# Optimization experiments

Measured on AMD Instinct MI355X. Metric: run time of the kernel, lower is better.

Reference implementation:

```python
import jax, jax.numpy as jnp
import numpy as np

H = 48       # query heads
KVH = 8      # kv heads (GQA)
G = H // KVH # groups = 6
D = 128      # head_dim
HID = 6144
ROPE_THETA = 1e6


def setup_inputs() -> dict:
    key = jax.random.key(0)
    k1, k2, k3 = jax.random.split(key, 3)
    x = jax.random.normal(k1, (2, 2048, HID), dtype=jnp.float32)
    Wqkv = jax.random.normal(k2, (8192, HID), dtype=jnp.float32) * 0.02
    Wo = jax.random.normal(k3, (HID, HID), dtype=jnp.float32) * 0.02
    return {"x": x, "Wqkv": Wqkv, "Wo": Wo}


def _rotate_half(u):
    return jnp.concatenate([-u[..., D // 2:], u[..., :D // 2]], axis=-1)


def reference(x, Wqkv, Wo):
    B, S, _ = x.shape
    # fused QKV projection, InternLM2 packed layout [B,S,KVH,2+G,D]
    qkv = jnp.einsum('bsh,oh->bso', x, Wqkv).reshape(B, S, KVH, G + 2, D)
    q = qkv[..., :G, :].reshape(B, S, H, D)   # [B,S,H,D]
    k = qkv[..., G, :]                        # [B,S,KVH,D]
    v = qkv[..., G + 1, :]                    # [B,S,KVH,D]

    # RoPE (rotate-half style, theta=1e6)
    inv_freq = 1.0 / (ROPE_THETA ** (jnp.arange(0, D, 2, dtype=jnp.float32) / D))
    freqs = jnp.outer(jnp.arange(S, dtype=jnp.float32), inv_freq)  # [S, D/2]
    emb = jnp.concatenate([freqs, freqs], axis=-1)                 # [S, D]
    cos = jnp.cos(emb)[None, :, None, :]
    sin = jnp.sin(emb)[None, :, None, :]
    q = q * cos + _rotate_half(q) * sin
    k = k * cos + _rotate_half(k) * sin

    # GQA: expand kv heads to query heads
    k = jnp.repeat(k, G, axis=2)  # [B,S,H,D]
    v = jnp.repeat(v, G, axis=2)

    scale = jnp.float32(1.0 / np.sqrt(D))
    scores = jnp.einsum('bqhd,bkhd->bhqk', q, k) * scale  # [B,H,S,S]
    causal = jnp.tril(jnp.ones((S, S), dtype=bool))
    scores = jnp.where(causal[None, None], scores, jnp.float32(-1e30))
    attn = jax.nn.softmax(scores, axis=-1)
    ctx = jnp.einsum('bhqk,bkhd->bqhd', attn, v).reshape(B, S, HID)
    return jnp.einsum('bsh,oh->bso', ctx, Wo)
```

## Files before the change

### kernel.cpp

```cpp
#include <hip/hip_runtime.h>
#include <stdint.h>
#include <stddef.h>


typedef unsigned short u16;
typedef __attribute__((ext_vector_type(8))) short short8;
typedef __attribute__((ext_vector_type(4))) float f32x4;
typedef __attribute__((ext_vector_type(4))) unsigned short u16x4;

typedef const __attribute__((address_space(1))) void* as1_cvp;
typedef __attribute__((address_space(3))) void* as3_vp;

__device__ __forceinline__ float bf2f(u16 u) {
  union { unsigned int i; float f; } v; v.i = ((unsigned)u) << 16; return v.f;
}
__device__ __forceinline__ u16 f2bf(float f) {
  union { float f; unsigned int i; } v; v.f = f;
  unsigned r = v.i + 0x7FFFu + ((v.i >> 16) & 1u);
  return (u16)(r >> 16);
}
__device__ __forceinline__ void gload_lds16(const void* g, void* l) {
  __builtin_amdgcn_global_load_lds((as1_cvp)g, (as3_vp)l, 16, 0, 0);
}

__global__ __launch_bounds__(256) void k_f2bf(const float* __restrict__ in,
                                              u16* __restrict__ out) {
  size_t i = ((size_t)blockIdx.x * 256 + threadIdx.x) * 4;
  f32x4 v = *(const f32x4*)(in + i);
  u16x4 o;
  o[0] = f2bf(v[0]); o[1] = f2bf(v[1]); o[2] = f2bf(v[2]); o[3] = f2bf(v[3]);
  *(u16x4*)(out + i) = o;
}

__device__ __forceinline__ void stage_region(const u16* __restrict__ G,
                                             int K, int kt,
                                             u16 (* __restrict__ XS)[64],
                                             int rmap, int w, int lane) {
  #pragma unroll
  for (int L = 0; L < 2; ++L) {
    const int g = w * 2 + L;
    int rb;
    if (rmap == 0)      rb = g * 8 + (g >> 3) * 64;
    else if (rmap == 1) rb = 64 + g * 8 + (g >> 3) * 64;
    else if (rmap == 2) rb = (g >> 2) * 64 + (g & 3) * 8;
    else                rb = 32 + (g >> 2) * 64 + (g & 3) * 8;
    const int srow = rb + (lane >> 3);
    const int schunk = ((lane & 7) ^ ((lane >> 3) & 7)) * 8;
    gload_lds16(G + (size_t)srow * K + (size_t)kt * 64 + schunk, &XS[rb][0]);
  }
}

#define LDFRAG(XS, row, ks) \
  (*(const short8*)&XS[row][(((ks) * 32) + lhi * 8) ^ swz])

#define MFMA_Q(af, bf, mb, nb)                                              \
  _Pragma("unroll") for (int mf = 0; mf < 4; ++mf)                          \
  _Pragma("unroll") for (int nf = 0; nf < 2; ++nf)                          \
  _Pragma("unroll") for (int ks = 0; ks < 2; ++ks)                          \
    acc[(mb) + mf][(nb) + nf] = __builtin_amdgcn_mfma_f32_16x16x32_bf16(    \
        af[mf][ks], bf[nf][ks], acc[(mb) + mf][(nb) + nf], 0, 0, 0);

#define GEMM_HALF(H) {                                                      \
  const int tAhi  = (t + 1 + (H) < nkt) ? (t + 1 + (H)) : (nkt - 1);        \
  const int tNext = (t + 2 + (H) < nkt) ? (t + 2 + (H)) : (nkt - 1);        \
  short8 a0[4][2], a1[4][2], b0[2][2], b1[2][2];                            \
                         \
  _Pragma("unroll") for (int mf = 0; mf < 4; ++mf) {                        \
    a0[mf][0] = LDFRAG(As[H], wm * 128 + mf * 16 + l16, 0);                 \
    a0[mf][1] = LDFRAG(As[H], wm * 128 + mf * 16 + l16, 1); }               \
  _Pragma("unroll") for (int nf = 0; nf < 2; ++nf) {                        \
    b0[nf][0] = LDFRAG(Bs[H], wn * 64 + nf * 16 + l16, 0);                  \
    b0[nf][1] = LDFRAG(Bs[H], wn * 64 + nf * 16 + l16, 1); }                \
  stage_region(Ap, K, tAhi, As[1 - (H)], 1, w, lane);                       \
  asm volatile("s_waitcnt lgkmcnt(8)" ::: "memory");                        \
  __builtin_amdgcn_s_barrier();                                             \
  asm volatile("s_waitcnt lgkmcnt(0)" ::: "memory");                        \
  __builtin_amdgcn_sched_barrier(0);                                        \
  __builtin_amdgcn_s_setprio(1);                                            \
  MFMA_Q(a0, b0, 0, 0);                                                     \
  __builtin_amdgcn_s_setprio(0);                                            \
  __builtin_amdgcn_s_barrier();                                             \
                          \
  _Pragma("unroll") for (int nf = 0; nf < 2; ++nf) {                        \
    b1[nf][0] = LDFRAG(Bs[H], wn * 64 + (nf + 2) * 16 + l16, 0);            \
    b1[nf][1] = LDFRAG(Bs[H], wn * 64 + (nf + 2) * 16 + l16, 1); }          \
  stage_region(Ap, K, tNext, As[H], 0, w, lane);                            \
  __builtin_amdgcn_s_barrier();                                             \
  asm volatile("s_waitcnt lgkmcnt(0)" ::: "memory");                        \
  __builtin_amdgcn_sched_barrier(0);                                        \
  __builtin_amdgcn_s_setprio(1);                                            \
  MFMA_Q(a0, b1, 0, 2);                                                     \
  __builtin_amdgcn_s_setprio(0);                                            \
  __builtin_amdgcn_s_barrier();                                             \
                          \
  _Pragma("unroll") for (int mf = 0; mf < 4; ++mf) {                        \
    a1[mf][0] = LDFRAG(As[H], wm * 128 + (mf + 4) * 16 + l16, 0);           \
    a1[mf][1] = LDFRAG(As[H], wm * 128 + (mf + 4) * 16 + l16, 1); }         \
  stage_region(Bp, K, tNext, Bs[H], 2, w, lane);                            \
  __builtin_amdgcn_s_barrier();                                             \
  asm volatile("s_waitcnt lgkmcnt(0)" ::: "memory");                        \
  __builtin_amdgcn_sched_barrier(0);                                        \
  __builtin_amdgcn_s_setprio(1);                                            \
  MFMA_Q(a1, b0, 4, 0);                                                     \
  __builtin_amdgcn_s_setprio(0);                                            \
  __builtin_amdgcn_s_barrier();                                             \
      \
  stage_region(Bp, K, tNext, Bs[H], 3, w, lane);                            \
  asm volatile("s_waitcnt vmcnt(6)" ::: "memory");                          \
  __builtin_amdgcn_s_barrier();                                             \
  __builtin_amdgcn_s_setprio(1);                                            \
  MFMA_Q(a1, b1, 4, 2);                                                     \
  __builtin_amdgcn_s_setprio(0);                                            \
  __builtin_amdgcn_s_barrier();                                             \
}

template<int WRITE_BF16>
__global__ __launch_bounds__(512, 2) void k_gemm256(const u16* __restrict__ A,
                                                    const u16* __restrict__ B,
                                                    void* __restrict__ Cout,
                                                    int M, int N, int K) {
  __shared__ u16 As[2][256][64];
  __shared__ u16 Bs[2][256][64];
  (void)M;
  const int tid  = threadIdx.x;
  const int lane = tid & 63;
  const int w    = tid >> 6;
  const int wm   = w >> 2;
  const int wn   = w & 3;
  const int l16  = lane & 15, lhi = lane >> 4;
  const int swz  = (l16 & 7) << 3;

  const int nbx = gridDim.x;
  int id = blockIdx.y * nbx + blockIdx.x;
  const int cpx = (nbx * gridDim.y) >> 3;
  id = (id & 7) * cpx + (id >> 3);
  const long m0 = (long)(id / nbx) * 256;
  const long n0 = (long)(id % nbx) * 256;

  const u16* Ap = A + (size_t)m0 * K;
  const u16* Bp = B + (size_t)n0 * K;

  f32x4 acc[8][4] = {};
  const int nkt = K >> 6;
  const int niter = nkt >> 1;

  stage_region(Ap, K, 0, As[0], 0, w, lane);
  stage_region(Ap, K, 0, As[0], 1, w, lane);
  stage_region(Bp, K, 0, Bs[0], 2, w, lane);
  stage_region(Bp, K, 0, Bs[0], 3, w, lane);
  stage_region(Ap, K, 1, As[1], 0, w, lane);
  stage_region(Bp, K, 1, Bs[1], 2, w, lane);
  stage_region(Bp, K, 1, Bs[1], 3, w, lane);
  asm volatile("s_waitcnt vmcnt(6)" ::: "memory");
  __builtin_amdgcn_s_barrier();

  for (int i = 0; i < niter; ++i) {
    const int t = 2 * i;
    GEMM_HALF(0)
    GEMM_HALF(1)
  }

  asm volatile("s_waitcnt vmcnt(0)" ::: "memory");
  #pragma unroll
  for (int mf = 0; mf < 8; ++mf)
    #pragma unroll
    for (int nf = 0; nf < 4; ++nf)
      #pragma unroll
      for (int j = 0; j < 4; ++j) {
        const size_t row = m0 + wm * 128 + mf * 16 + lhi * 4 + j;
        const size_t col = n0 + wn * 64 + nf * 16 + l16;
        const float v = acc[mf][nf][j];
        if (WRITE_BF16) ((u16*)Cout)[row * N + col] = f2bf(v);
        else            ((float*)Cout)[row * N + col] = v;
      }
}

__global__ __launch_bounds__(256) void k_rope(const u16* __restrict__ QKV,
                                              u16* __restrict__ Qo,
                                              u16* __restrict__ Ko) {
  const unsigned tid = blockIdx.x * 256 + threadIdx.x;
  const int j    = tid & 63;
  const int slot = (tid >> 6) & 7;
  const int kvh  = (tid >> 9) & 7;
  const int t    = tid >> 12;
  if (slot == 7) return;
  const int b = t >> 11, s = t & 2047;
  const size_t base = (size_t)t * 8192 + kvh * 1024 + slot * 128;
  const float v0 = bf2f(QKV[base + j]);
  const float v1 = bf2f(QKV[base + j + 64]);
  const float invf = __expf(-(float)j * 0.21586735246819181f);
  const float ang = (float)s * invf;
  float sn, cs;
  __sincosf(ang, &sn, &cs);
  const float o0 = v0 * cs - v1 * sn;
  const float o1 = v1 * cs + v0 * sn;
  if (slot < 6) {
    const int hh = kvh * 6 + slot;
    const size_t o = ((size_t)(b * 48 + hh) * 2048 + s) * 128 + j;
    Qo[o] = f2bf(o0); Qo[o + 64] = f2bf(o1);
  } else {
    const size_t o = ((size_t)(b * 8 + kvh) * 2048 + s) * 128 + j;
    Ko[o] = f2bf(o0); Ko[o + 64] = f2bf(o1);
  }
}

__global__ __launch_bounds__(256) void k_vtrans(const u16* __restrict__ QKV,
                                                u16* __restrict__ VT) {
  __shared__ u16 T[64][136];
  const int bid = blockIdx.x;
  const int st  = bid & 31;
  const int kvh = (bid >> 5) & 7;
  const int b   = bid >> 8;
  const int tid = threadIdx.x;
  const int r   = tid >> 4;
  const int c8  = (tid & 15) * 8;
  const size_t qoff = ((size_t)(b * 2048 + st * 64)) * 8192 + kvh * 1024 + 896;
  #pragma unroll
  for (int p = 0; p < 4; ++p) {
    short8 v = *(const short8*)&QKV[qoff + (size_t)(p * 16 + r) * 8192 + c8];
    *(short8*)&T[p * 16 + r][c8] = v;
  }
  __syncthreads();
  const int dd = tid >> 3;
  const int s8 = (tid & 7) * 8;
  const size_t vbase = ((size_t)(b * 8 + kvh) * 128) * 2048 + st * 64;
  #pragma unroll
  for (int p = 0; p < 4; ++p) {
    const int d = p * 32 + dd;
    short8 o;
    #pragma unroll
    for (int i = 0; i < 8; ++i) o[i] = (short)T[s8 + i][d];
    *(short8*)&VT[vbase + (size_t)d * 2048 + s8] = o;
  }
}

__global__ __launch_bounds__(256) void k_attn(const u16* __restrict__ Q,
                                              const u16* __restrict__ Kg,
                                              const u16* __restrict__ VT,
                                              u16* __restrict__ CTX) {
  __shared__ u16 Ks[64][128];
  __shared__ u16 Vs[128][64];
  __shared__ u16 Ps[4][16][64];
  const int bid = blockIdx.x;
  const int qt  = 31 - (bid / 96);
  const int bh  = bid % 96;
  const int h   = bh % 48;
  const int b   = bh / 48;
  const int kvh = h / 6;
  const int tid = threadIdx.x, lane = tid & 63, w = tid >> 6;
  const int l16 = lane & 15, lhi = lane >> 4;
  const int swz = (l16 & 7) << 3;
  const float SC = 0.08838834764831845f;

  short8 qf[4];
  {
    const size_t qrow = ((size_t)(b * 48 + h) * 2048 + qt * 64 + w * 16 + l16) * 128;
    #pragma unroll
    for (int kc = 0; kc < 4; ++kc)
      qf[kc] = *(const short8*)&Q[qrow + kc * 32 + lhi * 8];
  }
  f32x4 cacc[8] = {};
  float m_r[4], l_r[4];
  #pragma unroll
  for (int j = 0; j < 4; ++j) { m_r[j] = -1e30f; l_r[j] = 0.f; }

  const u16* Kb = Kg + (size_t)(b * 8 + kvh) * 2048 * 128;
  const u16* Vb = VT + (size_t)(b * 8 + kvh) * 128 * 2048;

  for (int kt = 0; kt <= qt; ++kt) {
    #pragma unroll
    for (int c = 0; c < 4; ++c) {
      const int krow = w * 16 + c * 4 + lhi;
      const int kcol = (l16 * 8) ^ ((krow & 7) << 3);
      gload_lds16(&Kb[(size_t)(kt * 64 + krow) * 128 + kcol], &Ks[w * 16 + c * 4][0]);
      const int vrow = w * 32 + c * 8 + (lane >> 3);
      const int vcol = ((lane & 7) * 8) ^ (((lane >> 3) & 7) << 3);
      gload_lds16(&Vb[(size_t)vrow * 2048 + kt * 64 + vcol], &Vs[w * 32 + c * 8][0]);
    }
    __syncthreads();

    f32x4 sacc[4] = {};
    #pragma unroll
    for (int ni = 0; ni < 4; ++ni)
      #pragma unroll
      for (int kc = 0; kc < 4; ++kc) {
        const short8 kfr = *(const short8*)&Ks[ni * 16 + l16][(kc * 32 + lhi * 8) ^ swz];
        sacc[ni] = __builtin_amdgcn_mfma_f32_16x16x32_bf16(qf[kc], kfr, sacc[ni], 0, 0, 0);
      }

    const bool diag = (kt == qt);
    float sv[4][4], alpha[4];
    #pragma unroll
    for (int j = 0; j < 4; ++j) {
      const int rloc = w * 16 + lhi * 4 + j;
      float mx = -1e30f;
      #pragma unroll
      for (int ni = 0; ni < 4; ++ni) {
        float s = sacc[ni][j] * SC;
        if (diag && (ni * 16 + l16 > rloc)) s = -1e30f;
        sv[ni][j] = s;
        mx = fmaxf(mx, s);
      }
      mx = fmaxf(mx, __shfl_xor(mx, 1, 16));
      mx = fmaxf(mx, __shfl_xor(mx, 2, 16));
      mx = fmaxf(mx, __shfl_xor(mx, 4, 16));
      mx = fmaxf(mx, __shfl_xor(mx, 8, 16));
      const float mnew = fmaxf(m_r[j], mx);
      alpha[j] = __expf(m_r[j] - mnew);
      float rs = 0.f;
      #pragma unroll
      for (int ni = 0; ni < 4; ++ni) {
        const float p = __expf(sv[ni][j] - mnew);
        sv[ni][j] = p;
        rs += p;
      }
      rs += __shfl_xor(rs, 1, 16);
      rs += __shfl_xor(rs, 2, 16);
      rs += __shfl_xor(rs, 4, 16);
      rs += __shfl_xor(rs, 8, 16);
      l_r[j] = l_r[j] * alpha[j] + rs;
      m_r[j] = mnew;
    }
    #pragma unroll
    for (int ni = 0; ni < 4; ++ni)
      #pragma unroll
      for (int j = 0; j < 4; ++j)
        Ps[w][lhi * 4 + j][(ni * 16 + l16) ^ (((lhi * 4 + j) & 7) << 3)] = f2bf(sv[ni][j]);
    #pragma unroll
    for (int nb = 0; nb < 8; ++nb)
      #pragma unroll
      for (int j = 0; j < 4; ++j)
        cacc[nb][j] *= alpha[j];
    #pragma unroll
    for (int kc2 = 0; kc2 < 2; ++kc2) {
      const short8 pa = *(const short8*)&Ps[w][l16][(kc2 * 32 + lhi * 8) ^ swz];
      #pragma unroll
      for (int nb = 0; nb < 8; ++nb) {
        const short8 vfr = *(const short8*)&Vs[nb * 16 + l16][(kc2 * 32 + lhi * 8) ^ swz];
        cacc[nb] = __builtin_amdgcn_mfma_f32_16x16x32_bf16(pa, vfr, cacc[nb], 0, 0, 0);
      }
    }
    __syncthreads();
  }

  const size_t crow = (size_t)(b * 2048 + qt * 64 + w * 16);
  #pragma unroll
  for (int nb = 0; nb < 8; ++nb)
    #pragma unroll
    for (int j = 0; j < 4; ++j) {
      const float v = cacc[nb][j] / l_r[j];
      CTX[(crow + lhi * 4 + j) * 6144 + h * 128 + nb * 16 + l16] = f2bf(v);
    }
}

extern "C" void kernel_launch(void* const* d_in, const int* in_sizes, int n_in,
                              void* d_out, int out_size, void* d_ws, size_t ws_size,
                              hipStream_t stream) {
  const float* x    = (const float*)d_in[0];
  const float* wqkv = (const float*)d_in[1];
  const float* wo   = (const float*)d_in[2];
  float* out = (float*)d_out;
  char* ws = (char*)d_ws;

  u16* xb  = (u16*)(ws);
  u16* wqb = (u16*)(ws + 50331648UL);
  u16* wob = (u16*)(ws + 150994944UL);
  u16* qkv = (u16*)(ws + 226492416UL);
  u16* Qb  = (u16*)(ws + 293601280UL);
  u16* Kb  = (u16*)(ws + 343932928UL);
  u16* VTb = (u16*)(ws + 352321536UL);
  u16* ctx = (u16*)(ws + 360710144UL);

  k_f2bf<<<25165824 / 1024, 256, 0, stream>>>(x, xb);
  k_f2bf<<<50331648 / 1024, 256, 0, stream>>>(wqkv, wqb);
  k_f2bf<<<37748736 / 1024, 256, 0, stream>>>(wo, wob);

  k_gemm256<1><<<dim3(8192 / 256, 4096 / 256), 512, 0, stream>>>(
      xb, wqb, qkv, 4096, 8192, 6144);

  k_rope<<<16777216 / 256, 256, 0, stream>>>(qkv, Qb, Kb);
  k_vtrans<<<512, 256, 0, stream>>>(qkv, VTb);

  k_attn<<<2 * 48 * 32, 256, 0, stream>>>(Qb, Kb, VTb, ctx);

  k_gemm256<0><<<dim3(6144 / 256, 4096 / 256), 512, 0, stream>>>(
      ctx, wob, out, 4096, 6144, 6144);
}
```

Before: 1.207 ms.

## Software-pipeline LDS fragment reads across GEMM half-iterations and drop barriers

The GEMM main loop now loads the next half's first A and B fragments from shared memory during the final MFMA quarter of the current half. Each remaining fragment read is moved one quarter earlier, so it overlaps the previous MFMA block. The extra s_barrier and explicit lgkmcnt waits between the read and MFMA phases are removed, and the fragment registers are hoisted out of the macro so they persist across iterations. The goal is to hide LDS read latency and cut synchronization stalls. In exchange, register pressure rises and correctness now depends on the existing vmcnt waits and barriers still ordering the async global-to-LDS staging.

```diff
diff --git a/kernel.cpp b/kernel.cpp
--- a/kernel.cpp
+++ b/kernel.cpp
@@ -60,54 +60,50 @@
     acc[(mb) + mf][(nb) + nf] = __builtin_amdgcn_mfma_f32_16x16x32_bf16(    \
         af[mf][ks], bf[nf][ks], acc[(mb) + mf][(nb) + nf], 0, 0, 0);
 
+#define READ_A(dst, XS, off)                                                \
+  _Pragma("unroll") for (int mf = 0; mf < 4; ++mf) {                        \
+    dst[mf][0] = LDFRAG(XS, wm * 128 + (mf + (off)) * 16 + l16, 0);         \
+    dst[mf][1] = LDFRAG(XS, wm * 128 + (mf + (off)) * 16 + l16, 1); }
+
+#define READ_B(dst, XS, off)                                                \
+  _Pragma("unroll") for (int nf = 0; nf < 2; ++nf) {                        \
+    dst[nf][0] = LDFRAG(XS, wn * 64 + (nf + (off)) * 16 + l16, 0);          \
+    dst[nf][1] = LDFRAG(XS, wn * 64 + (nf + (off)) * 16 + l16, 1); }
+
 #define GEMM_HALF(H) {                                                      \
   const int tAhi  = (t + 1 + (H) < nkt) ? (t + 1 + (H)) : (nkt - 1);        \
   const int tNext = (t + 2 + (H) < nkt) ? (t + 2 + (H)) : (nkt - 1);        \
-  short8 a0[4][2], a1[4][2], b0[2][2], b1[2][2];                            \
-                         \
-  _Pragma("unroll") for (int mf = 0; mf < 4; ++mf) {                        \
-    a0[mf][0] = LDFRAG(As[H], wm * 128 + mf * 16 + l16, 0);                 \
-    a0[mf][1] = LDFRAG(As[H], wm * 128 + mf * 16 + l16, 1); }               \
-  _Pragma("unroll") for (int nf = 0; nf < 2; ++nf) {                        \
-    b0[nf][0] = LDFRAG(Bs[H], wn * 64 + nf * 16 + l16, 0);                  \
-    b0[nf][1] = LDFRAG(Bs[H], wn * 64 + nf * 16 + l16, 1); }                \
+        \
+  READ_B(b1, Bs[H], 2);                                                     \
   stage_region(Ap, K, tAhi, As[1 - (H)], 1, w, lane);                       \
-  asm volatile("s_waitcnt lgkmcnt(8)" ::: "memory");                        \
-  __builtin_amdgcn_s_barrier();                                             \
-  asm volatile("s_waitcnt lgkmcnt(0)" ::: "memory");                        \
   __builtin_amdgcn_sched_barrier(0);                                        \
   __builtin_amdgcn_s_setprio(1);                                            \
   MFMA_Q(a0, b0, 0, 0);                                                     \
   __builtin_amdgcn_s_setprio(0);                                            \
   __builtin_amdgcn_s_barrier();                                             \
-                          \
-  _Pragma("unroll") for (int nf = 0; nf < 2; ++nf) {                        \
-    b1[nf][0] = LDFRAG(Bs[H], wn * 64 + (nf + 2) * 16 + l16, 0);            \
-    b1[nf][1] = LDFRAG(Bs[H], wn * 64 + (nf + 2) * 16 + l16, 1); }          \
+                                  \
+  READ_A(a1, As[H], 4);                                                     \
   stage_region(Ap, K, tNext, As[H], 0, w, lane);                            \
-  __builtin_amdgcn_s_barrier();                                             \
-  asm volatile("s_waitcnt lgkmcnt(0)" ::: "memory");                        \
   __builtin_amdgcn_sched_barrier(0);                                        \
   __builtin_amdgcn_s_setprio(1);                                            \
   MFMA_Q(a0, b1, 0, 2);                                                     \
   __builtin_amdgcn_s_setprio(0);                                            \
   __builtin_amdgcn_s_barrier();                                             \
-                          \
-  _Pragma("unroll") for (int mf = 0; mf < 4; ++mf) {                        \
-    a1[mf][0] = LDFRAG(As[H], wm * 128 + (mf + 4) * 16 + l16, 0);           \
-    a1[mf][1] = LDFRAG(As[H], wm * 128 + (mf + 4) * 16 + l16, 1); }         \
+                                           \
   stage_region(Bp, K, tNext, Bs[H], 2, w, lane);                            \
-  __builtin_amdgcn_s_barrier();                                             \
-  asm volatile("s_waitcnt lgkmcnt(0)" ::: "memory");                        \
   __builtin_amdgcn_sched_barrier(0);                                        \
   __builtin_amdgcn_s_setprio(1);                                            \
   MFMA_Q(a1, b0, 4, 0);                                                     \
   __builtin_amdgcn_s_setprio(0);                                            \
   __builtin_amdgcn_s_barrier();                                             \
-      \
+  \
+             \
   stage_region(Bp, K, tNext, Bs[H], 3, w, lane);                            \
   asm volatile("s_waitcnt vmcnt(6)" ::: "memory");                          \
   __builtin_amdgcn_s_barrier();                                             \
+  READ_A(a0, As[1 - (H)], 0);                                               \
+  READ_B(b0, Bs[1 - (H)], 0);                                               \
+  __builtin_amdgcn_sched_barrier(0);                                        \
   __builtin_amdgcn_s_setprio(1);                                            \
   MFMA_Q(a1, b1, 4, 2);                                                     \
   __builtin_amdgcn_s_setprio(0);                                            \
@@ -141,6 +137,7 @@
   const u16* Bp = B + (size_t)n0 * K;
 
   f32x4 acc[8][4] = {};
+  short8 a0[4][2], a1[4][2], b0[2][2], b1[2][2];
   const int nkt = K >> 6;
   const int niter = nkt >> 1;
 
@@ -153,6 +150,8 @@
   stage_region(Bp, K, 1, Bs[1], 3, w, lane);
   asm volatile("s_waitcnt vmcnt(6)" ::: "memory");
   __builtin_amdgcn_s_barrier();
+  READ_A(a0, As[0], 0);
+  READ_B(b0, Bs[0], 0);
 
   for (int i = 0; i < niter; ++i) {
     const int t = 2 * i;
```

Result: slower. 1.575 ms (+30.5%).
